# Kernel tuning notes

Hardware: AMD Instinct MI355X
Metric: run time of the kernel (lower is better)

Reference implementation:

```python
import jax, jax.numpy as jnp
import numpy as np

NUM_CAPS = 16      # num_capsules K
DIM_CAPS = 16      # dim_capsule Dc (output last dim is K*Dc per original tf.matmul quirk)
ROUTINGS = 3
EPS = 1e-7         # tf.keras.backend.epsilon()


def squash(v):
    # v: [..., d]
    sq = jnp.sum(v * v, axis=-1, keepdims=True)
    return (sq / (1.0 + sq)) * (v / jnp.sqrt(sq + EPS))


def setup_inputs() -> dict:
    key = jax.random.key(0)
    k1, k2 = jax.random.split(key)
    B, N, Din = 16, 1024, 512
    KD = NUM_CAPS * DIM_CAPS  # 256
    inputs = jax.random.normal(k1, (B, N, Din), dtype=jnp.float32)
    # glorot_uniform for W [Din, K*Dc]
    limit = float(np.sqrt(6.0 / (Din + KD)))
    W = jax.random.uniform(k2, (Din, KD), minval=-limit, maxval=limit, dtype=jnp.float32)
    return {"inputs": inputs, "W": W}


def reference(inputs, W):
    # Original: input_hat[b,n,k,:] = inputs[b,n,:] @ W  (tile over k is redundant)
    h = inputs @ W  # [B, N, K*Dc]
    B, N, _ = inputs.shape
    b = jnp.zeros((B, N, NUM_CAPS), dtype=inputs.dtype)
    out = None
    for i in range(ROUTINGS):
        c = jax.nn.softmax(b, axis=2)                      # [B, N, K]
        # sum_n c[b,n,k] * input_hat[b,n,k,d] == sum_n c[b,n,k] * h[b,n,d]
        s = jnp.einsum('bnk,bnd->bkd', c, h)               # [B, K, K*Dc]
        out = squash(s)                                    # [B, K, K*Dc]
        if i < ROUTINGS - 1:
            # agreement: sum_d input_hat[b,n,k,d] * out[b,k,d]
            b = b + jnp.einsum('bnd,bkd->bnk', h, out)
    return out  # [B, K, K*Dc] == tf.squeeze(outputs, axis=1)
```

## Files before the change

### kernel.cpp

```cpp
#include <hip/hip_runtime.h>

#define BSZ    16
#define NN     1024
#define DIN    512
#define KD     256
#define NCAPS  16
#define EPS    1e-7f

#define ROWS_PER_BLK 32
#define NCHUNK (NN / ROWS_PER_BLK)
#define NSPLIT 16
#define ICHUNK (DIN / NSPLIT)


__global__ __launch_bounds__(256) void colsum_partial(
    const float* __restrict__ in, float* __restrict__ P)
{
    __shared__ float4 sh[128];
    int blk = blockIdx.x;
    int t   = threadIdx.x;
    int par  = t >> 7;
    int col4 = t & 127;

    const float4* base = (const float4*)in
        + (size_t)blk * ROWS_PER_BLK * (DIN / 4);

    float4 acc = make_float4(0.f, 0.f, 0.f, 0.f);
    #pragma unroll
    for (int r = 0; r < ROWS_PER_BLK / 2; ++r) {
        float4 v = base[(size_t)(2 * r + par) * (DIN / 4) + col4];
        acc.x += v.x; acc.y += v.y; acc.z += v.z; acc.w += v.w;
    }
    if (par) sh[col4] = acc;
    __syncthreads();
    if (!par) {
        float4 o = sh[col4];
        acc.x += o.x; acc.y += o.y; acc.z += o.z; acc.w += o.w;
        ((float4*)P)[(size_t)blk * (DIN / 4) + col4] = acc;
    }
}

__global__ __launch_bounds__(256) void partial_gemm(
    const float* __restrict__ P, const float* __restrict__ W,
    float* __restrict__ P2)
{
    __shared__ float wl[ICHUNK][KD];
    __shared__ float pt[ICHUNK][33];
    __shared__ float pr[8][33];
    __shared__ float xs[ICHUNK];

    const int b  = blockIdx.x >> 4;
    const int s  = blockIdx.x & (NSPLIT - 1);
    const int t  = threadIdx.x;
    const int i0 = s * ICHUNK;

    const float4* W4 = (const float4*)W + (size_t)i0 * (KD / 4);
    float4 wv[8];
    #pragma unroll
    for (int k = 0; k < 8; ++k)
        wv[k] = W4[k * 256 + t];

    const int c = t >> 3;
    const int q = t & 7;
    float4 pv = ((const float4*)P)[((size_t)b * NCHUNK + c) * (DIN / 4)
                                   + (i0 / 4) + q];

    #pragma unroll
    for (int k = 0; k < 8; ++k) {
        int idx  = k * 256 + t;
        int row  = idx >> 6;
        int col4 = idx & 63;
        *(float4*)&wl[row][col4 * 4] = wv[k];
    }
    pt[c][q * 4 + 0] = pv.x;
    pt[c][q * 4 + 1] = pv.y;
    pt[c][q * 4 + 2] = pv.z;
    pt[c][q * 4 + 3] = pv.w;
    __syncthreads();

    {
        const int g = t >> 5;
        const int i = t & 31;
        pr[g][i] = pt[g * 4 + 0][i] + pt[g * 4 + 1][i]
                 + pt[g * 4 + 2][i] + pt[g * 4 + 3][i];
    }
    __syncthreads();
    if (t < ICHUNK)
        xs[t] = pr[0][t] + pr[1][t] + pr[2][t] + pr[3][t]
              + pr[4][t] + pr[5][t] + pr[6][t] + pr[7][t];
    __syncthreads();

    float acc = 0.f;
    #pragma unroll
    for (int i = 0; i < ICHUNK; ++i)
        acc += xs[i] * wl[i][t];
    P2[((size_t)b * NSPLIT + s) * KD + t] = acc;
}

__global__ __launch_bounds__(256) void squash_out(
    const float* __restrict__ P2, float* __restrict__ out)
{
    __shared__ float part[4][KD];
    __shared__ float svs[KD];
    __shared__ float red[KD];

    const int b = blockIdx.x;
    const int t = threadIdx.x;
    const int g  = t >> 6;
    const int d4 = t & 63;

    const float4* P24 = (const float4*)P2 + (size_t)b * NSPLIT * (KD / 4);
    float4 a = make_float4(0.f, 0.f, 0.f, 0.f);
    #pragma unroll
    for (int j = 0; j < 4; ++j) {
        float4 v = P24[(size_t)(g * 4 + j) * (KD / 4) + d4];
        a.x += v.x; a.y += v.y; a.z += v.z; a.w += v.w;
    }
    *(float4*)&part[g][d4 * 4] = a;
    __syncthreads();

    const float sv = (part[0][t] + part[1][t] + part[2][t] + part[3][t])
                     * (1.0f / 16.0f);
    svs[t] = sv;
    red[t] = sv * sv;
    __syncthreads();
    for (int off = 128; off > 0; off >>= 1) {
        if (t < off) red[t] += red[t + off];
        __syncthreads();
    }
    const float sq    = red[0];
    const float scale = (sq / (1.0f + sq)) / sqrtf(sq + EPS);
    const float o     = scale * svs[t];

    #pragma unroll
    for (int k = 0; k < NCAPS; ++k)
        out[((size_t)b * NCAPS + k) * KD + t] = o;
}

extern "C" void kernel_launch(void* const* d_in, const int* in_sizes, int n_in,
                              void* d_out, int out_size, void* d_ws, size_t ws_size,
                              hipStream_t stream)
{
    const float* in = (const float*)d_in[0];
    const float* W  = (const float*)d_in[1];
    float* out = (float*)d_out;

    float* P  = (float*)d_ws;
    float* P2 = P + (size_t)BSZ * NCHUNK * DIN;

    colsum_partial<<<BSZ * NCHUNK, 256, 0, stream>>>(in, P);
    partial_gemm<<<BSZ * NSPLIT, 256, 0, stream>>>(P, W, P2);
    squash_out<<<BSZ, 256, 0, stream>>>(P2, out);
}
```

Before: 15.10 us.

## Fuse column-sum reduction into partial GEMM kernel, dropping one launch

Merges the column-sum kernel and the partial GEMM into one kernel. Each of 512 blocks sums 512 rows of a 32-column slice of the input and multiplies that sum by the matching W slice. This removes a kernel launch and the round trip of the partial-sum buffer through global memory, and squash_out now reduces 32 partials instead of 16. In exchange the grid shrinks from 1024 to 512 blocks for streaming 32 MB of input, and each thread reads a narrow 128-byte column strip with a large row stride, which may reduce memory-level parallelism.

```diff
diff --git a/kernel.cpp b/kernel.cpp
--- a/kernel.cpp
+++ b/kernel.cpp
@@ -7,63 +7,47 @@
 #define NCAPS  16
 #define EPS    1e-7f
 
-#define ROWS_PER_BLK 32
-#define NCHUNK (NN / ROWS_PER_BLK)
-#define NSPLIT 16
-#define ICHUNK (DIN / NSPLIT)
+#define NSPLIT  16
+#define ICHUNK  (DIN / NSPLIT)
+#define NHALF   2
+#define NPART   (NSPLIT * NHALF)
 
-
-__global__ __launch_bounds__(256) void colsum_partial(
-    const float* __restrict__ in, float* __restrict__ P)
-{
-    __shared__ float4 sh[128];
-    int blk = blockIdx.x;
-    int t   = threadIdx.x;
-    int par  = t >> 7;
-    int col4 = t & 127;
-
-    const float4* base = (const float4*)in
-        + (size_t)blk * ROWS_PER_BLK * (DIN / 4);
-
-    float4 acc = make_float4(0.f, 0.f, 0.f, 0.f);
-    #pragma unroll
-    for (int r = 0; r < ROWS_PER_BLK / 2; ++r) {
-        float4 v = base[(size_t)(2 * r + par) * (DIN / 4) + col4];
-        acc.x += v.x; acc.y += v.y; acc.z += v.z; acc.w += v.w;
-    }
-    if (par) sh[col4] = acc;
-    __syncthreads();
-    if (!par) {
-        float4 o = sh[col4];
-        acc.x += o.x; acc.y += o.y; acc.z += o.z; acc.w += o.w;
-        ((float4*)P)[(size_t)blk * (DIN / 4) + col4] = acc;
-    }
-}
-
-__global__ __launch_bounds__(256) void partial_gemm(
-    const float* __restrict__ P, const float* __restrict__ W,
+__global__ __launch_bounds__(256, 2) void colsum_gemm(
+    const float* __restrict__ in, const float* __restrict__ W,
     float* __restrict__ P2)
 {
-    __shared__ float wl[ICHUNK][KD];
-    __shared__ float pt[ICHUNK][33];
-    __shared__ float pr[8][33];
-    __shared__ float xs[ICHUNK];
+    __shared__ float  wl[ICHUNK][KD];
+    __shared__ float4 shp[32][8];
+    __shared__ float4 pr[8][8];
+    __shared__ float  xs[ICHUNK];
 
-    const int b  = blockIdx.x >> 4;
-    const int s  = blockIdx.x & (NSPLIT - 1);
-    const int t  = threadIdx.x;
-    const int i0 = s * ICHUNK;
+    const int blk  = blockIdx.x;
+    const int b    = blk >> 5;
+    const int r5   = blk & 31;
+    const int s    = r5 >> 1;
+    const int half = r5 & 1;
+    const int t    = threadIdx.x;
 
-    const float4* W4 = (const float4*)W + (size_t)i0 * (KD / 4);
+    const float4* W4 = (const float4*)W + (size_t)(s * ICHUNK) * (KD / 4);
     float4 wv[8];
     #pragma unroll
     for (int k = 0; k < 8; ++k)
         wv[k] = W4[k * 256 + t];
 
-    const int c = t >> 3;
-    const int q = t & 7;
-    float4 pv = ((const float4*)P)[((size_t)b * NCHUNK + c) * (DIN / 4)
-                                   + (i0 / 4) + q];
+    {
+        const int rg = t >> 3;
+        const int c4 = t & 7;
+        const float4* base = (const float4*)in
+            + ((size_t)(b * NN + half * 512) * (DIN / 4))
+            + (size_t)s * (ICHUNK / 4) + c4;
+        float4 a = make_float4(0.f, 0.f, 0.f, 0.f);
+        #pragma unroll
+        for (int j = 0; j < 16; ++j) {
+            float4 v = base[(size_t)(rg + 32 * j) * (DIN / 4)];
+            a.x += v.x; a.y += v.y; a.z += v.z; a.w += v.w;
+        }
+        shp[rg][c4] = a;
+    }
 
     #pragma unroll
     for (int k = 0; k < 8; ++k) {
@@ -72,29 +56,36 @@
         int col4 = idx & 63;
         *(float4*)&wl[row][col4 * 4] = wv[k];
     }
-    pt[c][q * 4 + 0] = pv.x;
-    pt[c][q * 4 + 1] = pv.y;
-    pt[c][q * 4 + 2] = pv.z;
-    pt[c][q * 4 + 3] = pv.w;
     __syncthreads();
 
-    {
-        const int g = t >> 5;
-        const int i = t & 31;
-        pr[g][i] = pt[g * 4 + 0][i] + pt[g * 4 + 1][i]
-                 + pt[g * 4 + 2][i] + pt[g * 4 + 3][i];
+    if (t < 64) {
+        const int rg2 = t >> 3;
+        const int c4  = t & 7;
+        float4 a = shp[rg2 * 4 + 0][c4];
+        #pragma unroll
+        for (int u = 1; u < 4; ++u) {
+            float4 v = shp[rg2 * 4 + u][c4];
+            a.x += v.x; a.y += v.y; a.z += v.z; a.w += v.w;
+        }
+        pr[rg2][c4] = a;
     }
     __syncthreads();
-    if (t < ICHUNK)
-        xs[t] = pr[0][t] + pr[1][t] + pr[2][t] + pr[3][t]
-              + pr[4][t] + pr[5][t] + pr[6][t] + pr[7][t];
+    if (t < 8) {
+        float4 a = pr[0][t];
+        #pragma unroll
+        for (int u = 1; u < 8; ++u) {
+            float4 v = pr[u][t];
+            a.x += v.x; a.y += v.y; a.z += v.z; a.w += v.w;
+        }
+        *(float4*)&xs[t * 4] = a;
+    }
     __syncthreads();
 
     float acc = 0.f;
     #pragma unroll
     for (int i = 0; i < ICHUNK; ++i)
         acc += xs[i] * wl[i][t];
-    P2[((size_t)b * NSPLIT + s) * KD + t] = acc;
+    P2[((size_t)b * NPART + r5) * KD + t] = acc;
 }
 
 __global__ __launch_bounds__(256) void squash_out(
@@ -109,11 +100,11 @@
     const int g  = t >> 6;
     const int d4 = t & 63;
 
-    const float4* P24 = (const float4*)P2 + (size_t)b * NSPLIT * (KD / 4);
+    const float4* P24 = (const float4*)P2 + (size_t)b * NPART * (KD / 4);
     float4 a = make_float4(0.f, 0.f, 0.f, 0.f);
     #pragma unroll
-    for (int j = 0; j < 4; ++j) {
-        float4 v = P24[(size_t)(g * 4 + j) * (KD / 4) + d4];
+    for (int j = 0; j < 8; ++j) {
+        float4 v = P24[(size_t)(g * 8 + j) * (KD / 4) + d4];
         a.x += v.x; a.y += v.y; a.z += v.z; a.w += v.w;
     }
     *(float4*)&part[g][d4 * 4] = a;
@@ -145,10 +136,8 @@
     const float* W  = (const float*)d_in[1];
     float* out = (float*)d_out;
 
-    float* P  = (float*)d_ws;
-    float* P2 = P + (size_t)BSZ * NCHUNK * DIN;
+    float* P2 = (float*)d_ws;
 
-    colsum_partial<<<BSZ * NCHUNK, 256, 0, stream>>>(in, P);
-    partial_gemm<<<BSZ * NSPLIT, 256, 0, stream>>>(P, W, P2);
+    colsum_gemm<<<BSZ * NPART, 256, 0, stream>>>(in, W, P2);
     squash_out<<<BSZ, 256, 0, stream>>>(P2, out);
 }
```

Result: faster. 12.96 us (-14.1%).
